# Kernel optimization log

Measured on AMD Instinct MI355X. Metric: run time of the kernel, lower is better.

The kernel has to match this reference:

```python
import jax, jax.numpy as jnp
import numpy as np

N = 35          # nodes (hardcoded by x.repeat(35,1,1))
V = 4           # edge views
D1, D2, D3 = 512, 256, 128


def _full_graph_edges():
    # fully connected, no self loops, COO [2, E], E = 35*34
    src, dst = np.meshgrid(np.arange(N), np.arange(N), indexing='ij')
    mask = src != dst
    return np.stack([src[mask], dst[mask]], axis=0).astype(np.int64)


def setup_inputs() -> dict:
    key = jax.random.key(0)
    ks = jax.random.split(key, 8)
    E = N * (N - 1)
    edge_index = jnp.asarray(_full_graph_edges())
    s1, s2, s3 = 1.0 / np.sqrt(V), 1.0 / np.sqrt(V), 1.0 / np.sqrt(V)
    return {
        'x': jnp.ones((N, 1), jnp.float32),
        'edge_attr': jax.random.uniform(ks[0], (E, V), jnp.float32),
        'edge_index': edge_index,
        'mlp1_w': jax.random.normal(ks[1], (V, 1 * D1), jnp.float32) * s1,
        'mlp1_b': jnp.zeros((1 * D1,), jnp.float32),
        'root1': jax.random.normal(ks[2], (1, D1), jnp.float32),
        'bias1': jnp.zeros((D1,), jnp.float32),
        'mlp2_w': jax.random.normal(ks[3], (V, D1 * D2), jnp.float32) * s2,
        'mlp2_b': jnp.zeros((D1 * D2,), jnp.float32),
        'root2': jax.random.normal(ks[4], (D1, D2), jnp.float32) / np.sqrt(D1),
        'bias2': jnp.zeros((D2,), jnp.float32),
        'mlp3_w': jax.random.normal(ks[5], (V, D2 * D3), jnp.float32) * s3,
        'mlp3_b': jnp.zeros((D2 * D3,), jnp.float32),
        'root3': jax.random.normal(ks[6], (D2, D3), jnp.float32) / np.sqrt(D2),
        'bias3': jnp.zeros((D3,), jnp.float32),
    }


def _nnconv(x, edge_attr, src, dst, mlp_w, mlp_b, root, bias, in_c, out_c):
    # edge MLP -> per-edge weight matrix [E, in_c, out_c]
    w = jax.nn.relu(edge_attr @ mlp_w + mlp_b).reshape(-1, in_c, out_c)
    # gather source feats, per-edge matmul: [E, out_c]
    msg = jnp.einsum('ei,eio->eo', x[src], w)
    # scatter-mean to targets
    agg = jax.ops.segment_sum(msg, dst, num_segments=N)
    cnt = jax.ops.segment_sum(jnp.ones_like(msg[:, 0]), dst, num_segments=N)
    agg = agg / jnp.maximum(cnt, 1.0)[:, None]
    return agg + x @ root + bias


def reference(x, edge_attr, edge_index, mlp1_w, mlp1_b, root1, bias1,
              mlp2_w, mlp2_b, root2, bias2, mlp3_w, mlp3_b, root3, bias3):
    src, dst = edge_index[0], edge_index[1]
    h = jax.nn.relu(_nnconv(x, edge_attr, src, dst, mlp1_w, mlp1_b, root1, bias1, 1, D1))
    h = jax.nn.relu(_nnconv(h, edge_attr, src, dst, mlp2_w, mlp2_b, root2, bias2, D1, D2))
    h = jax.nn.relu(_nnconv(h, edge_attr, src, dst, mlp3_w, mlp3_b, root3, bias3, D2, D3))
    # cbt[a, i] = sum_f |h[i, f] - h[a, f]|   (repeat / transpose / abs / sum)
    cbt = jnp.sum(jnp.abs(h[None, :, :] - h[:, None, :]), axis=2)
    return cbt
```

## Files before the change

### kernel.cpp

```cpp
#include <hip/hip_runtime.h>

#define NN 35

typedef float v2f __attribute__((ext_vector_type(2)));

__device__ __forceinline__ v2f pk_fma(v2f a, v2f b, v2f c) {
#if __has_builtin(__builtin_elementwise_fma)
    return __builtin_elementwise_fma(a, b, c);
#else
    v2f d; d.x = fmaf(a.x, b.x, c.x); d.y = fmaf(a.y, b.y, c.y); return d;
#endif
}
__device__ __forceinline__ v2f pk_relu(v2f a) {
    v2f d; d.x = fmaxf(a.x, 0.f); d.y = fmaxf(a.y, 0.f); return d;
}
__device__ __forceinline__ v2f pk_splat(float s) { v2f d; d.x = s; d.y = s; return d; }
__device__ __forceinline__ v2f pk_make(float a, float b) { v2f d; d.x = a; d.y = b; return d; }


__global__ __launch_bounds__(512)
void layer1_kernel(const float* __restrict__ x,
                   const float* __restrict__ ea,
                   const float* __restrict__ W1, const float* __restrict__ b1,
                   const float* __restrict__ root1, const float* __restrict__ bias1,
                   float* __restrict__ h1,
                   float* __restrict__ aggz)
{
    const int d = blockIdx.x;
    const int o = threadIdx.x;
    const int gtid = d * 512 + o;
    if (gtid < 35 * 384) aggz[gtid] = 0.f;

    const float w0 = W1[o], w1 = W1[512 + o], w2 = W1[1024 + o], w3 = W1[1536 + o];
    const float bb = b1[o];
    float sum = 0.f;
#pragma unroll
    for (int s = 0; s < NN; ++s) {
        if (s == d) continue;
        const float4 a = ((const float4*)ea)[s * 34 + (d < s ? d : d - 1)];
        float w = fmaf(a.x, w0, fmaf(a.y, w1, fmaf(a.z, w2, fmaf(a.w, w3, bb))));
        sum = fmaf(x[s], fmaxf(w, 0.f), sum);
    }
    h1[gtid] = fmaxf(sum * (1.f / 34.f) + x[d] * root1[o] + bias1[o], 0.f);
}

__global__ __launch_bounds__(256, 2)
void edge2_kernel(const float* __restrict__ h,
                  const float* __restrict__ ea,
                  const float* __restrict__ W,
                  const float* __restrict__ bias,
                  const float* __restrict__ root,
                  float* __restrict__ agg)
{
    const int d  = blockIdx.x;
    const int c  = blockIdx.y;
    const int i0 = c * 8;
    const int o  = threadIdx.x;

    __shared__ __align__(16) float hs[35][8];
    __shared__ float4 as[34];

    v2f Wv0[4], Wv1[4], Wv2[4], Wv3[4], BB[4], RR[4];
#pragma unroll
    for (int p = 0; p < 4; ++p) {
        const size_t b0 = (size_t)(i0 + 2 * p) * 256 + o;
        const size_t bq = b0 + 256;
        Wv0[p] = pk_make(W[b0],          W[bq]);
        Wv1[p] = pk_make(W[131072 + b0], W[131072 + bq]);
        Wv2[p] = pk_make(W[262144 + b0], W[262144 + bq]);
        Wv3[p] = pk_make(W[393216 + b0], W[393216 + bq]);
        BB[p]  = pk_make(bias[b0],       bias[bq]);
        RR[p]  = pk_make(root[b0],       root[bq]);
    }

    if (o < 70) {
        const int r = o >> 1, k = o & 1;
        const int s = (r < 34) ? (r + (r >= d ? 1 : 0)) : d;
        ((float4*)hs[r])[k] = ((const float4*)(h + (size_t)s * 512 + i0))[k];
    }
    if (o >= 70 && o < 104) {
        const int j = o - 70;
        const int s = j + (j >= d ? 1 : 0);
        as[j] = ((const float4*)ea)[s * 34 + (d < s ? d : d - 1)];
    }
    __syncthreads();

    v2f acc0 = pk_splat(0.f), acc1 = pk_splat(0.f);
#pragma unroll 2
    for (int j = 0; j < 34; ++j) {
        const float4 a = as[j];
        const v2f ax = pk_splat(a.x), ay = pk_splat(a.y);
        const v2f az = pk_splat(a.z), aw = pk_splat(a.w);
#pragma unroll
        for (int k = 0; k < 2; ++k) {
            const float4 hv = ((const float4*)hs[j])[k];
            {
                const int p = k * 2;
                v2f w = pk_fma(ax, Wv0[p], pk_fma(ay, Wv1[p],
                        pk_fma(az, Wv2[p], pk_fma(aw, Wv3[p], BB[p]))));
                acc0 = pk_fma(pk_make(hv.x, hv.y), pk_relu(w), acc0);
            }
            {
                const int p = k * 2 + 1;
                v2f w = pk_fma(ax, Wv0[p], pk_fma(ay, Wv1[p],
                        pk_fma(az, Wv2[p], pk_fma(aw, Wv3[p], BB[p]))));
                acc1 = pk_fma(pk_make(hv.z, hv.w), pk_relu(w), acc1);
            }
        }
    }
    v2f racc = pk_splat(0.f);
#pragma unroll
    for (int k = 0; k < 2; ++k) {
        const float4 hv = ((const float4*)hs[34])[k];
        racc = pk_fma(pk_make(hv.x, hv.y), RR[k * 2],     racc);
        racc = pk_fma(pk_make(hv.z, hv.w), RR[k * 2 + 1], racc);
    }
    const float acc = acc0.x + acc0.y + acc1.x + acc1.y;
    atomicAdd(&agg[d * 256 + o], acc * (1.f / 34.f) + (racc.x + racc.y));
}

__global__ __launch_bounds__(256, 2)
void edge3_kernel(const float* __restrict__ agg2,
                  const float* __restrict__ bias2,
                  const float* __restrict__ ea,
                  const float* __restrict__ W,
                  const float* __restrict__ bias,
                  const float* __restrict__ root,
                  float* __restrict__ agg)
{
    const int d   = blockIdx.x;
    const int c   = blockIdx.y;
    const int i0  = c * 8;
    const int thr = threadIdx.x;
    const int o   = thr & 127;
    const int g   = thr >> 7;

    __shared__ __align__(16) float hs[35][8];
    __shared__ float4 as[34];

    v2f Wv0[2], Wv1[2], Wv2[2], Wv3[2], BB[2], RR[2];
#pragma unroll
    for (int p = 0; p < 2; ++p) {
        const size_t b0 = (size_t)(i0 + g * 4 + 2 * p) * 128 + o;
        const size_t bq = b0 + 128;
        Wv0[p] = pk_make(W[b0],         W[bq]);
        Wv1[p] = pk_make(W[32768 + b0], W[32768 + bq]);
        Wv2[p] = pk_make(W[65536 + b0], W[65536 + bq]);
        Wv3[p] = pk_make(W[98304 + b0], W[98304 + bq]);
        BB[p]  = pk_make(bias[b0],      bias[bq]);
        RR[p]  = pk_make(root[b0],      root[bq]);
    }

    if (thr < 70) {
        const int r = thr >> 1, k = thr & 1;
        const int s = (r < 34) ? (r + (r >= d ? 1 : 0)) : d;
        float4 v = ((const float4*)(agg2 + (size_t)s * 256 + i0))[k];
        const float4 bv = ((const float4*)(bias2 + i0))[k];
        v.x = fmaxf(v.x + bv.x, 0.f);
        v.y = fmaxf(v.y + bv.y, 0.f);
        v.z = fmaxf(v.z + bv.z, 0.f);
        v.w = fmaxf(v.w + bv.w, 0.f);
        ((float4*)hs[r])[k] = v;
    }
    if (thr >= 70 && thr < 104) {
        const int j = thr - 70;
        const int s = j + (j >= d ? 1 : 0);
        as[j] = ((const float4*)ea)[s * 34 + (d < s ? d : d - 1)];
    }
    __syncthreads();

    v2f acc0 = pk_splat(0.f), acc1 = pk_splat(0.f);
#pragma unroll 2
    for (int j = 0; j < 34; ++j) {
        const float4 a = as[j];
        const v2f ax = pk_splat(a.x), ay = pk_splat(a.y);
        const v2f az = pk_splat(a.z), aw = pk_splat(a.w);
        const float4 hv = ((const float4*)hs[j])[g];
        {
            v2f w = pk_fma(ax, Wv0[0], pk_fma(ay, Wv1[0],
                    pk_fma(az, Wv2[0], pk_fma(aw, Wv3[0], BB[0]))));
            acc0 = pk_fma(pk_make(hv.x, hv.y), pk_relu(w), acc0);
        }
        {
            v2f w = pk_fma(ax, Wv0[1], pk_fma(ay, Wv1[1],
                    pk_fma(az, Wv2[1], pk_fma(aw, Wv3[1], BB[1]))));
            acc1 = pk_fma(pk_make(hv.z, hv.w), pk_relu(w), acc1);
        }
    }
    v2f racc = pk_splat(0.f);
    {
        const float4 hv = ((const float4*)hs[34])[g];
        racc = pk_fma(pk_make(hv.x, hv.y), RR[0], racc);
        racc = pk_fma(pk_make(hv.z, hv.w), RR[1], racc);
    }
    const float acc = acc0.x + acc0.y + acc1.x + acc1.y;
    atomicAdd(&agg[d * 128 + o], acc * (1.f / 34.f) + (racc.x + racc.y));
}

__global__ __launch_bounds__(256)
void cbt_kernel(const float* __restrict__ agg3,
                const float* __restrict__ bias3,
                float* __restrict__ out)
{
    const int wv = blockIdx.x * 4 + (threadIdx.x >> 6);
    const int lane = threadIdx.x & 63;
    if (wv >= NN * NN) return;
    const int a_ = wv / NN, i_ = wv % NN;
    float s = 0.f;
#pragma unroll
    for (int q = 0; q < 2; ++q) {
        const int f = lane + q * 64;
        const float bb = bias3[f];
        const float hi = fmaxf(agg3[i_ * 128 + f] + bb, 0.f);
        const float ha = fmaxf(agg3[a_ * 128 + f] + bb, 0.f);
        s += fabsf(hi - ha);
    }
#pragma unroll
    for (int off = 32; off > 0; off >>= 1)
        s += __shfl_xor(s, off, 64);
    if (lane == 0) out[wv] = s;
}

extern "C" void kernel_launch(void* const* d_in, const int* in_sizes, int n_in,
                              void* d_out, int out_size, void* d_ws, size_t ws_size,
                              hipStream_t stream) {
    const float* x      = (const float*)d_in[0];
    const float* ea     = (const float*)d_in[1];
    const float* mlp1_w = (const float*)d_in[3];
    const float* mlp1_b = (const float*)d_in[4];
    const float* root1  = (const float*)d_in[5];
    const float* bias1  = (const float*)d_in[6];
    const float* mlp2_w = (const float*)d_in[7];
    const float* mlp2_b = (const float*)d_in[8];
    const float* root2  = (const float*)d_in[9];
    const float* bias2  = (const float*)d_in[10];
    const float* mlp3_w = (const float*)d_in[11];
    const float* mlp3_b = (const float*)d_in[12];
    const float* root3  = (const float*)d_in[13];
    const float* bias3  = (const float*)d_in[14];
    float* out = (float*)d_out;

    float* ws   = (float*)d_ws;
    float* agg2 = ws;
    float* agg3 = agg2 + 35 * 256;
    float* h1   = agg3 + 35 * 128;

    layer1_kernel<<<NN, 512, 0, stream>>>(x, ea, mlp1_w, mlp1_b, root1, bias1, h1, agg2);
    edge2_kernel<<<dim3(NN, 64), 256, 0, stream>>>(h1, ea, mlp2_w, mlp2_b, root2, agg2);
    edge3_kernel<<<dim3(NN, 32), 256, 0, stream>>>(agg2, bias2, ea, mlp3_w, mlp3_b, root3, agg3);
    cbt_kernel<<<(NN * NN + 3) / 4, 256, 0, stream>>>(agg3, bias3, out);
}
```

Measured before the change: 128.4 us.

## Fuse layer-1 into edge2 and replace layer-2 atomics with partial-sum buffer

Removes the separate layer-1 kernel. Each edge2 block now recomputes the layer-1 features for its 8-channel slice of all 35 nodes in shared memory. Layer-2 results go to a per-chunk partial buffer instead of atomicAdd, and edge3 sums those 64 partials while staging its inputs. This cuts one launch and atomic contention, and zeroes agg3 inside the fused kernel. In exchange, every block redoes layer-1 work and edge3 reads a larger partial buffer.

```diff
diff --git a/kernel.cpp b/kernel.cpp
--- a/kernel.cpp
+++ b/kernel.cpp
@@ -17,67 +17,50 @@
 __device__ __forceinline__ v2f pk_splat(float s) { v2f d; d.x = s; d.y = s; return d; }
 __device__ __forceinline__ v2f pk_make(float a, float b) { v2f d; d.x = a; d.y = b; return d; }
 
-
-__global__ __launch_bounds__(512)
-void layer1_kernel(const float* __restrict__ x,
+__device__ __forceinline__ void agst(float* p, float v) {
+    __hip_atomic_store(p, v, __ATOMIC_RELAXED, __HIP_MEMORY_SCOPE_AGENT);
+}
+
+
+__global__ __launch_bounds__(256, 2)
+void edge12_kernel(const float* __restrict__ x,
                    const float* __restrict__ ea,
                    const float* __restrict__ W1, const float* __restrict__ b1,
                    const float* __restrict__ root1, const float* __restrict__ bias1,
-                   float* __restrict__ h1,
-                   float* __restrict__ aggz)
-{
-    const int d = blockIdx.x;
-    const int o = threadIdx.x;
-    const int gtid = d * 512 + o;
-    if (gtid < 35 * 384) aggz[gtid] = 0.f;
-
-    const float w0 = W1[o], w1 = W1[512 + o], w2 = W1[1024 + o], w3 = W1[1536 + o];
-    const float bb = b1[o];
-    float sum = 0.f;
-#pragma unroll
-    for (int s = 0; s < NN; ++s) {
-        if (s == d) continue;
-        const float4 a = ((const float4*)ea)[s * 34 + (d < s ? d : d - 1)];
-        float w = fmaf(a.x, w0, fmaf(a.y, w1, fmaf(a.z, w2, fmaf(a.w, w3, bb))));
-        sum = fmaf(x[s], fmaxf(w, 0.f), sum);
-    }
-    h1[gtid] = fmaxf(sum * (1.f / 34.f) + x[d] * root1[o] + bias1[o], 0.f);
-}
-
-__global__ __launch_bounds__(256, 2)
-void edge2_kernel(const float* __restrict__ h,
-                  const float* __restrict__ ea,
-                  const float* __restrict__ W,
-                  const float* __restrict__ bias,
-                  const float* __restrict__ root,
-                  float* __restrict__ agg)
+                   const float* __restrict__ W2, const float* __restrict__ b2,
+                   const float* __restrict__ root2,
+                   float* __restrict__ part,
+                   float* __restrict__ agg3)
 {
     const int d  = blockIdx.x;
     const int c  = blockIdx.y;
     const int i0 = c * 8;
     const int o  = threadIdx.x;
+    const int bid = c * 35 + d;
 
     __shared__ __align__(16) float hs[35][8];
     __shared__ float4 as[34];
+    __shared__ float xs[NN];
+
+    if (bid < 18) {
+        const int zi = bid * 256 + o;
+        if (zi < 35 * 128) agst(&agg3[zi], 0.f);
+    }
 
     v2f Wv0[4], Wv1[4], Wv2[4], Wv3[4], BB[4], RR[4];
 #pragma unroll
     for (int p = 0; p < 4; ++p) {
         const size_t b0 = (size_t)(i0 + 2 * p) * 256 + o;
         const size_t bq = b0 + 256;
-        Wv0[p] = pk_make(W[b0],          W[bq]);
-        Wv1[p] = pk_make(W[131072 + b0], W[131072 + bq]);
-        Wv2[p] = pk_make(W[262144 + b0], W[262144 + bq]);
-        Wv3[p] = pk_make(W[393216 + b0], W[393216 + bq]);
-        BB[p]  = pk_make(bias[b0],       bias[bq]);
-        RR[p]  = pk_make(root[b0],       root[bq]);
-    }
-
-    if (o < 70) {
-        const int r = o >> 1, k = o & 1;
-        const int s = (r < 34) ? (r + (r >= d ? 1 : 0)) : d;
-        ((float4*)hs[r])[k] = ((const float4*)(h + (size_t)s * 512 + i0))[k];
-    }
+        Wv0[p] = pk_make(W2[b0],          W2[bq]);
+        Wv1[p] = pk_make(W2[131072 + b0], W2[131072 + bq]);
+        Wv2[p] = pk_make(W2[262144 + b0], W2[262144 + bq]);
+        Wv3[p] = pk_make(W2[393216 + b0], W2[393216 + bq]);
+        BB[p]  = pk_make(b2[b0],          b2[bq]);
+        RR[p]  = pk_make(root2[b0],       root2[bq]);
+    }
+
+    if (o < NN) xs[o] = x[o];
     if (o >= 70 && o < 104) {
         const int j = o - 70;
         const int s = j + (j >= d ? 1 : 0);
@@ -85,15 +68,32 @@
     }
     __syncthreads();
 
+    for (int e = o; e < 280; e += 256) {
+        const int s = e >> 3, ii = e & 7, i = i0 + ii;
+        const float w0 = W1[i], w1 = W1[512 + i], w2 = W1[1024 + i], w3 = W1[1536 + i];
+        const float bb = b1[i];
+        float sum = 0.f;
+#pragma unroll
+        for (int t = 0; t < NN; ++t) {
+            if (t == s) continue;
+            const float4 a = ((const float4*)ea)[t * 34 + (s < t ? s : s - 1)];
+            float w = fmaf(a.x, w0, fmaf(a.y, w1, fmaf(a.z, w2, fmaf(a.w, w3, bb))));
+            sum = fmaf(xs[t], fmaxf(w, 0.f), sum);
+        }
+        hs[s][ii] = fmaxf(sum * (1.f / 34.f) + xs[s] * root1[i] + bias1[i], 0.f);
+    }
+    __syncthreads();
+
     v2f acc0 = pk_splat(0.f), acc1 = pk_splat(0.f);
 #pragma unroll 2
     for (int j = 0; j < 34; ++j) {
+        const int sj = j + (j >= d ? 1 : 0);
         const float4 a = as[j];
         const v2f ax = pk_splat(a.x), ay = pk_splat(a.y);
         const v2f az = pk_splat(a.z), aw = pk_splat(a.w);
 #pragma unroll
         for (int k = 0; k < 2; ++k) {
-            const float4 hv = ((const float4*)hs[j])[k];
+            const float4 hv = ((const float4*)hs[sj])[k];
             {
                 const int p = k * 2;
                 v2f w = pk_fma(ax, Wv0[p], pk_fma(ay, Wv1[p],
@@ -111,16 +111,16 @@
     v2f racc = pk_splat(0.f);
 #pragma unroll
     for (int k = 0; k < 2; ++k) {
-        const float4 hv = ((const float4*)hs[34])[k];
+        const float4 hv = ((const float4*)hs[d])[k];
         racc = pk_fma(pk_make(hv.x, hv.y), RR[k * 2],     racc);
         racc = pk_fma(pk_make(hv.z, hv.w), RR[k * 2 + 1], racc);
     }
     const float acc = acc0.x + acc0.y + acc1.x + acc1.y;
-    atomicAdd(&agg[d * 256 + o], acc * (1.f / 34.f) + (racc.x + racc.y));
+    part[((size_t)(d * 256 + o) << 6) + c] = acc * (1.f / 34.f) + (racc.x + racc.y);
 }
 
 __global__ __launch_bounds__(256, 2)
-void edge3_kernel(const float* __restrict__ agg2,
+void edge3_kernel(const float* __restrict__ part,
                   const float* __restrict__ bias2,
                   const float* __restrict__ ea,
                   const float* __restrict__ W,
@@ -151,31 +151,37 @@
         RR[p]  = pk_make(root[b0],      root[bq]);
     }
 
-    if (thr < 70) {
-        const int r = thr >> 1, k = thr & 1;
-        const int s = (r < 34) ? (r + (r >= d ? 1 : 0)) : d;
-        float4 v = ((const float4*)(agg2 + (size_t)s * 256 + i0))[k];
-        const float4 bv = ((const float4*)(bias2 + i0))[k];
-        v.x = fmaxf(v.x + bv.x, 0.f);
-        v.y = fmaxf(v.y + bv.y, 0.f);
-        v.z = fmaxf(v.z + bv.z, 0.f);
-        v.w = fmaxf(v.w + bv.w, 0.f);
-        ((float4*)hs[r])[k] = v;
-    }
-    if (thr >= 70 && thr < 104) {
-        const int j = thr - 70;
-        const int s = j + (j >= d ? 1 : 0);
-        as[j] = ((const float4*)ea)[s * 34 + (d < s ? d : d - 1)];
+    if (thr < 34) {
+        const int s = thr + (thr >= d ? 1 : 0);
+        as[thr] = ((const float4*)ea)[s * 34 + (d < s ? d : d - 1)];
+    }
+
+    for (int e = thr; e < 280; e += 256) {
+        const int s = e >> 3, f = i0 + (e & 7);
+        const float4* pp = (const float4*)(part + ((size_t)(s * 256 + f) << 6));
+        float4 v0 = pp[0], v1 = pp[1], v2 = pp[2], v3 = pp[3];
+#pragma unroll
+        for (int q = 4; q < 16; q += 4) {
+            const float4 a0 = pp[q], a1 = pp[q + 1], a2 = pp[q + 2], a3 = pp[q + 3];
+            v0.x += a0.x; v0.y += a0.y; v0.z += a0.z; v0.w += a0.w;
+            v1.x += a1.x; v1.y += a1.y; v1.z += a1.z; v1.w += a1.w;
+            v2.x += a2.x; v2.y += a2.y; v2.z += a2.z; v2.w += a2.w;
+            v3.x += a3.x; v3.y += a3.y; v3.z += a3.z; v3.w += a3.w;
+        }
+        const float v = (v0.x + v0.y + v0.z + v0.w) + (v1.x + v1.y + v1.z + v1.w)
+                      + (v2.x + v2.y + v2.z + v2.w) + (v3.x + v3.y + v3.z + v3.w);
+        hs[s][e & 7] = fmaxf(v + bias2[f], 0.f);
     }
     __syncthreads();
 
     v2f acc0 = pk_splat(0.f), acc1 = pk_splat(0.f);
 #pragma unroll 2
     for (int j = 0; j < 34; ++j) {
+        const int sj = j + (j >= d ? 1 : 0);
         const float4 a = as[j];
         const v2f ax = pk_splat(a.x), ay = pk_splat(a.y);
         const v2f az = pk_splat(a.z), aw = pk_splat(a.w);
-        const float4 hv = ((const float4*)hs[j])[g];
+        const float4 hv = ((const float4*)hs[sj])[g];
         {
             v2f w = pk_fma(ax, Wv0[0], pk_fma(ay, Wv1[0],
                     pk_fma(az, Wv2[0], pk_fma(aw, Wv3[0], BB[0]))));
@@ -189,7 +195,7 @@
     }
     v2f racc = pk_splat(0.f);
     {
-        const float4 hv = ((const float4*)hs[34])[g];
+        const float4 hv = ((const float4*)hs[d])[g];
         racc = pk_fma(pk_make(hv.x, hv.y), RR[0], racc);
         racc = pk_fma(pk_make(hv.z, hv.w), RR[1], racc);
     }
@@ -241,12 +247,12 @@
     float* out = (float*)d_out;
 
     float* ws   = (float*)d_ws;
-    float* agg2 = ws;
-    float* agg3 = agg2 + 35 * 256;
-    float* h1   = agg3 + 35 * 128;
-
-    layer1_kernel<<<NN, 512, 0, stream>>>(x, ea, mlp1_w, mlp1_b, root1, bias1, h1, agg2);
-    edge2_kernel<<<dim3(NN, 64), 256, 0, stream>>>(h1, ea, mlp2_w, mlp2_b, root2, agg2);
-    edge3_kernel<<<dim3(NN, 32), 256, 0, stream>>>(agg2, bias2, ea, mlp3_w, mlp3_b, root3, agg3);
+    float* part = ws;
+    float* agg3 = ws + 573440;
+
+    edge12_kernel<<<dim3(NN, 64), 256, 0, stream>>>(
+        x, ea, mlp1_w, mlp1_b, root1, bias1, mlp2_w, mlp2_b, root2, part, agg3);
+    edge3_kernel<<<dim3(NN, 32), 256, 0, stream>>>(
+        part, bias2, ea, mlp3_w, mlp3_b, root3, agg3);
     cbt_kernel<<<(NN * NN + 3) / 4, 256, 0, stream>>>(agg3, bias3, out);
 }
```

Result: slower. 153.8 us (+19.8%).
